# Kernel tuning notes

Measured on AMD Instinct MI355X. Metric: run time of the kernel, lower is better.

Reference implementation:

```python
import jax, jax.numpy as jnp
import numpy as np

EPS = 1e-5

def setup_inputs() -> dict:
    key = jax.random.key(0)
    ks = jax.random.split(key, 4)
    B, C, H, W = 32, 256, 32, 32
    x = jax.random.normal(ks[0], (B, C, H, W), dtype=jnp.float32)
    gamma = jnp.ones((C,), dtype=jnp.float32)
    beta = jnp.zeros((C,), dtype=jnp.float32)
    # torch nn.Linear init scale ~ 1/sqrt(fan_in)
    W_kqv = jax.random.normal(ks[1], (3 * C, C), dtype=jnp.float32) / np.sqrt(C)
    b_kqv = jnp.zeros((3 * C,), dtype=jnp.float32)
    W_proj = jax.random.normal(ks[2], (C, C), dtype=jnp.float32) / np.sqrt(C)
    b_proj = jnp.zeros((C,), dtype=jnp.float32)
    return {"x": x, "gamma": gamma, "beta": beta, "W_kqv": W_kqv,
            "b_kqv": b_kqv, "W_proj": W_proj, "b_proj": b_proj}

def reference(x, gamma, beta, W_kqv, b_kqv, W_proj, b_proj):
    B, C, H, W = x.shape
    scale = jnp.sqrt(jnp.asarray(C, dtype=x.dtype))
    # BatchNorm2d (training-mode batch statistics, biased variance, eps=1e-5)
    mean = jnp.mean(x, axis=(0, 2, 3), keepdims=True)
    var = jnp.var(x, axis=(0, 2, 3), keepdims=True)
    t = (x - mean) * jax.lax.rsqrt(var + EPS)
    t = t * gamma[None, :, None, None] + beta[None, :, None, None]
    # [B, C, H, W] -> [B, N, C] with N = H*W
    t = t.reshape(B, C, H * W).transpose(0, 2, 1)
    kqv = t @ W_kqv.T + b_kqv           # [B, N, 3C]
    q, k, v = jnp.split(kqv, 3, axis=-1)  # each [B, N, C]
    s = jnp.einsum('bnc,bmc->bnm', q, k) / scale  # [B, N, N]
    attn = jax.nn.softmax(s, axis=-1)
    o = jnp.einsum('bnm,bmc->bnc', attn, v)        # [B, N, C]
    o = o @ W_proj.T + b_proj
    o = o.transpose(0, 2, 1).reshape(B, C, H, W)
    return o + x
```

## Files before the change

kernel.cpp:

```cpp
#include <hip/hip_runtime.h>

typedef unsigned short u16;
typedef __attribute__((ext_vector_type(8))) short bf16x8;
typedef __attribute__((ext_vector_type(4))) float f32x4;

__device__ __forceinline__ float bf2f(u16 u) {
  union { unsigned u; float f; } c; c.u = ((unsigned)u) << 16; return c.f;
}
__device__ __forceinline__ u16 f2bf(float f) {
  union { float f; unsigned u; } c; c.f = f;
  unsigned u = c.u;
  return (u16)((u + 0x7FFFu + ((u >> 16) & 1u)) >> 16);
}
__device__ __forceinline__ void gld16(const void* g, void* l) {
  __builtin_amdgcn_global_load_lds(
      (__attribute__((address_space(1))) void*)g,
      (__attribute__((address_space(3))) void*)l, 16, 0, 0);
}

#define SYNCB() do { \
  asm volatile("s_waitcnt vmcnt(0) lgkmcnt(0)" ::: "memory"); \
  __builtin_amdgcn_s_barrier(); \
  __builtin_amdgcn_sched_barrier(0); \
} while (0)

#define BB 32
#define CC 256
#define NN 1024

__global__ __launch_bounds__(256) void bn_stats_kernel(
    const float* __restrict__ x, const float* __restrict__ gamma,
    const float* __restrict__ beta, float* __restrict__ scl, float* __restrict__ sft)
{
  int c = blockIdx.x;
  int tid = threadIdx.x;
  float s = 0.f, q = 0.f;
  for (int g = tid; g < 8192; g += 256) {
    int b = g >> 8;
    int n = (g & 255) * 4;
    float4 v = *reinterpret_cast<const float4*>(x + (((size_t)(b * CC + c)) << 10) + n);
    s += v.x + v.y + v.z + v.w;
    q += v.x * v.x + v.y * v.y + v.z * v.z + v.w * v.w;
  }
  __shared__ float rs[256], rq[256];
  rs[tid] = s; rq[tid] = q;
  __syncthreads();
  for (int off = 128; off > 0; off >>= 1) {
    if (tid < off) { rs[tid] += rs[tid + off]; rq[tid] += rq[tid + off]; }
    __syncthreads();
  }
  if (tid == 0) {
    float mean = rs[0] * (1.f / 32768.f);
    float var  = rq[0] * (1.f / 32768.f) - mean * mean;
    float rstd = rsqrtf(var + 1e-5f);
    float g = gamma[c] * rstd;
    scl[c] = g;
    sft[c] = beta[c] - mean * g;
  }
}

__global__ __launch_bounds__(256) void prep_w_kernel(
    const float* __restrict__ Wk, const float* __restrict__ bk,
    const float* __restrict__ Wp, const float* __restrict__ bp,
    const float* __restrict__ scl, const float* __restrict__ sft,
    u16* __restrict__ Wkb, float* __restrict__ bkbf,
    u16* __restrict__ Wpb, float* __restrict__ bpbf)
{
  int o = blockIdx.x, c = threadIdx.x;
  __shared__ float red[256];
  if (o < 768) {
    float w = Wk[o * 256 + c];
    Wkb[o * 256 + c] = f2bf(w * scl[c]);
    red[c] = w * sft[c];
    __syncthreads();
    for (int off = 128; off > 0; off >>= 1) {
      if (c < off) red[c] += red[c + off];
      __syncthreads();
    }
    if (c == 0) bkbf[o] = bk[o] + red[0];
  } else {
    int op = o - 768;
    Wpb[op * 256 + c] = f2bf(Wp[op * 256 + c]);
    if (c == 0) bpbf[op] = bp[op];
  }
}

__global__ __launch_bounds__(256, 2) void qkv_fused_kernel(
    const float* __restrict__ x, const u16* __restrict__ Wkb,
    const float* __restrict__ bkbf, u16* __restrict__ qkout, u16* __restrict__ vt)
{
  __shared__ __align__(16) u16 As[2][128 * 32];
  __shared__ __align__(16) u16 Bs[2][256 * 32];
  int bid = blockIdx.x;
  int bx = bid & 255, by = bid >> 8;
  int b = bx >> 3, nsp0 = (bx & 7) * 128;
  int tid = threadIdx.x, lane = tid & 63, w = tid >> 6;
  int lq = lane & 15, quad = lane >> 4;
  int wm = (w >> 1) * 64, wn = (w & 1) * 128;
  int ar = lane >> 2, ac = (lane & 3) * 8;
  int rbB = w * 64;
  int nn4 = (tid & 31) * 4;
  int c8i = tid >> 5;
  int cg  = c8i * 4;

  const float* xb = x + (((size_t)(b * CC)) << 10) + nsp0 + nn4;
  const u16* Bw = Wkb + (size_t)(by * 256) * 256;

  f32x4 zero = {0.f, 0.f, 0.f, 0.f};
  f32x4 acc[4][8];
  #pragma unroll
  for (int i = 0; i < 4; ++i)
    #pragma unroll
    for (int j = 0; j < 8; ++j) acc[i][j] = zero;

  float4 xA[4], xB[4];
  #pragma unroll
  for (int i = 0; i < 4; ++i)
    gld16(Bw + (size_t)(rbB + i * 16 + ar) * 256 + ac, &Bs[0][(rbB + i * 16) * 32]);
  #pragma unroll
  for (int ci = 0; ci < 4; ++ci)
    xA[ci] = *reinterpret_cast<const float4*>(xb + ((size_t)(cg + ci) << 10));

  auto body = [&](int t, float4 (&xc)[4], float4 (&xn)[4]) {
    int k0 = t * 32;
    if (t < 7) {
      int kn = k0 + 32;
      #pragma unroll
      for (int i = 0; i < 4; ++i)
        gld16(Bw + (size_t)(rbB + i * 16 + ar) * 256 + kn + ac,
              &Bs[(t + 1) & 1][(rbB + i * 16) * 32]);
      #pragma unroll
      for (int ci = 0; ci < 4; ++ci)
        xn[ci] = *reinterpret_cast<const float4*>(xb + ((size_t)(kn + cg + ci) << 10));
    }
    if (t < 7) {
      asm volatile("s_waitcnt vmcnt(8)" ::: "memory");
    } else {
      asm volatile("s_waitcnt vmcnt(0)" ::: "memory");
    }
    __builtin_amdgcn_sched_barrier(0);
    u16 av[4][4];
    #pragma unroll
    for (int ci = 0; ci < 4; ++ci) {
      av[ci][0] = f2bf(xc[ci].x);
      av[ci][1] = f2bf(xc[ci].y);
      av[ci][2] = f2bf(xc[ci].z);
      av[ci][3] = f2bf(xc[ci].w);
    }
    int c16 = c8i >> 1, lo8 = (c8i & 1) * 4;
    #pragma unroll
    for (int ni = 0; ni < 4; ++ni) {
      int n = nn4 + ni;
      int s2 = (n >> 2) & 3;
      ushort4 o4;
      o4.x = av[0][ni]; o4.y = av[1][ni]; o4.z = av[2][ni]; o4.w = av[3][ni];
      *reinterpret_cast<ushort4*>(
          &As[t & 1][n * 32 + ((c16 ^ s2) * 8 + lo8)]) = o4;
    }
    asm volatile("s_waitcnt lgkmcnt(0)" ::: "memory");
    __builtin_amdgcn_s_barrier();
    __builtin_amdgcn_sched_barrier(0);

    bf16x8 af[4], bfr[8];
    #pragma unroll
    for (int i = 0; i < 4; ++i) {
      int r = wm + i * 16 + lq;
      af[i] = *reinterpret_cast<const bf16x8*>(
          &As[t & 1][r * 32 + ((quad ^ ((r >> 2) & 3)) * 8)]);
    }
    #pragma unroll
    for (int j = 0; j < 8; ++j)
      bfr[j] = *reinterpret_cast<const bf16x8*>(
          &Bs[t & 1][(wn + j * 16 + lq) * 32 + quad * 8]);
    __builtin_amdgcn_s_setprio(1);
    #pragma unroll
    for (int i = 0; i < 4; ++i)
      #pragma unroll
      for (int j = 0; j < 8; ++j)
        acc[i][j] = __builtin_amdgcn_mfma_f32_16x16x32_bf16(af[i], bfr[j], acc[i][j], 0, 0, 0);
    __builtin_amdgcn_s_setprio(0);
    asm volatile("s_waitcnt lgkmcnt(0)" ::: "memory");
    __builtin_amdgcn_s_barrier();
    __builtin_amdgcn_sched_barrier(0);
  };

  #pragma unroll 1
  for (int tt = 0; tt < 4; ++tt) {
    body(2 * tt,     xA, xB);
    body(2 * tt + 1, xB, xA);
  }

  if (by < 2) {
    #pragma unroll
    for (int j = 0; j < 8; ++j) {
      int col = by * 256 + wn + j * 16 + lq;
      float bv = bkbf[col];
      #pragma unroll
      for (int i = 0; i < 4; ++i) {
        int m = (b << 10) + nsp0 + wm + i * 16 + quad * 4;
        #pragma unroll
        for (int r = 0; r < 4; ++r)
          qkout[(size_t)(m + r) * 512 + col] = f2bf(acc[i][j][r] + bv);
      }
    }
  } else {
    #pragma unroll
    for (int j = 0; j < 8; ++j) {
      int col = wn + j * 16 + lq;
      float bv = bkbf[512 + col];
      #pragma unroll
      for (int i = 0; i < 4; ++i) {
        int n = nsp0 + wm + i * 16 + quad * 4;
        ushort4 o;
        o.x = f2bf(acc[i][j][0] + bv);
        o.y = f2bf(acc[i][j][1] + bv);
        o.z = f2bf(acc[i][j][2] + bv);
        o.w = f2bf(acc[i][j][3] + bv);
        *reinterpret_cast<ushort4*>(&vt[(size_t)b * 262144 + (size_t)col * 1024 + n]) = o;
      }
    }
  }
}

__global__ __launch_bounds__(256) void gemm_nt_kernel(
    const u16* __restrict__ A, int lda, size_t sA,
    const u16* __restrict__ B, int ldb, size_t sB,
    u16* __restrict__ C, int ldc, size_t sC,
    int K, const float* __restrict__ bias, float scale, int mode,
    const float* __restrict__ xres, float* __restrict__ outf)
{
  __shared__ u16 As[128 * 32];
  __shared__ u16 Bs[128 * 32];
  int tid = threadIdx.x;
  int m0 = blockIdx.x * 128, n0 = blockIdx.y * 128;
  const u16* Ab = A + (size_t)blockIdx.z * sA;
  const u16* Bb = B + (size_t)blockIdx.z * sB;
  u16* Cb = C + (size_t)blockIdx.z * sC;

  int lane = tid & 63, w = tid >> 6;
  int lq = lane & 15, quad = lane >> 4;
  int wm = (w >> 1) * 64, wn = (w & 1) * 64;
  int ar = lane >> 2, ac = (lane & 3) * 8;
  int rb = w * 32;

  f32x4 zero = {0.f, 0.f, 0.f, 0.f};
  f32x4 acc[4][4];
  #pragma unroll
  for (int i = 0; i < 4; ++i)
    #pragma unroll
    for (int j = 0; j < 4; ++j) acc[i][j] = zero;

  for (int k0 = 0; k0 < K; k0 += 32) {
    __syncthreads();
    gld16(Ab + (size_t)(m0 + rb +      ar) * lda + k0 + ac, &As[(rb     ) * 32]);
    gld16(Ab + (size_t)(m0 + rb + 16 + ar) * lda + k0 + ac, &As[(rb + 16) * 32]);
    gld16(Bb + (size_t)(n0 + rb +      ar) * ldb + k0 + ac, &Bs[(rb     ) * 32]);
    gld16(Bb + (size_t)(n0 + rb + 16 + ar) * ldb + k0 + ac, &Bs[(rb + 16) * 32]);
    __syncthreads();
    bf16x8 af[4], bfr[4];
    #pragma unroll
    for (int i = 0; i < 4; ++i) {
      af[i]  = *reinterpret_cast<const bf16x8*>(&As[(wm + i * 16 + lq) * 32 + quad * 8]);
      bfr[i] = *reinterpret_cast<const bf16x8*>(&Bs[(wn + i * 16 + lq) * 32 + quad * 8]);
    }
    #pragma unroll
    for (int i = 0; i < 4; ++i)
      #pragma unroll
      for (int j = 0; j < 4; ++j)
        acc[i][j] = __builtin_amdgcn_mfma_f32_16x16x32_bf16(af[i], bfr[j], acc[i][j], 0, 0, 0);
  }

  #pragma unroll
  for (int j = 0; j < 4; ++j) {
    int col = n0 + wn + j * 16 + lq;
    float bv = bias ? bias[col] : 0.f;
    #pragma unroll
    for (int i = 0; i < 4; ++i) {
      int rbase = m0 + wm + i * 16 + quad * 4;
      if (mode == 2) {
        int b = rbase >> 10, n = rbase & 1023;
        size_t idx = (((size_t)(b * CC + col)) << 10) + n;
        float4 xv = *reinterpret_cast<const float4*>(xres + idx);
        float4 o;
        o.x = acc[i][j][0] * scale + bv + xv.x;
        o.y = acc[i][j][1] * scale + bv + xv.y;
        o.z = acc[i][j][2] * scale + bv + xv.z;
        o.w = acc[i][j][3] * scale + bv + xv.w;
        *reinterpret_cast<float4*>(outf + idx) = o;
      } else {
        #pragma unroll
        for (int r = 0; r < 4; ++r)
          Cb[(size_t)(rbase + r) * ldc + col] = f2bf(acc[i][j][r] * scale + bv);
      }
    }
  }
}

__global__ __launch_bounds__(512, 2) void attn_kernel(
    const u16* __restrict__ qk,
    const u16* __restrict__ vt,
    u16* __restrict__ o)
{
  __shared__ __align__(16) u16 Ks[2][64 * 256];
  __shared__ __align__(16) u16 Vs[2][256 * 64];
  __shared__ __align__(16) u16 Ps[128 * 64];
  float* rs = (float*)Ps;

  int bid = blockIdx.x;
  int b  = (bid & 7) + 8 * ((bid >> 3) & 3);
  int qt = bid >> 5;
  int tid = threadIdx.x, lane = tid & 63, w = tid >> 6;
  int lq = lane & 15, hh = lane >> 4;
  int wr = w & 3;
  bool isQK = w < 4;

  const u16* qb = qk + ((size_t)b << 10) * 512;
  const u16* kb = qb + 256;
  const u16* vb = vt + ((size_t)b << 18);

  auto stageK = [&](int kt, int bufi) {
    #pragma unroll
    for (int i = 0; i < 4; ++i) {
      int slot = i * 512 + tid;
      int r = slot >> 5, c = slot & 31;
      gld16(kb + (size_t)(kt * 64 + r) * 512 + ((c ^ (r & 7)) << 3),
            &Ks[bufi][(i * 512 + (tid & 448)) * 8]);
    }
  };
  auto stageV = [&](int kt, int bufi) {
    #pragma unroll
    for (int i = 0; i < 4; ++i) {
      int slot = i * 512 + tid;
      int n = slot >> 3, c = slot & 7;
      gld16(vb + (size_t)(n << 10) + kt * 64 + ((c ^ (n & 7)) << 3),
            &Vs[bufi][(i * 512 + (tid & 448)) * 8]);
    }
  };

  f32x4 zero = {0.f, 0.f, 0.f, 0.f};

  stageK(0, 0);
  SYNCB();

  if (isQK) {
    int q0 = qt * 128 + wr * 32;
    bf16x8 qf[2][8];
    #pragma unroll
    for (int qi = 0; qi < 2; ++qi)
      #pragma unroll
      for (int kk = 0; kk < 8; ++kk)
        qf[qi][kk] = *reinterpret_cast<const bf16x8*>(
            qb + (size_t)(q0 + qi * 16 + lq) * 512 + kk * 32 + hh * 8);
    float runsum[2][4] = {{0.f, 0.f, 0.f, 0.f}, {0.f, 0.f, 0.f, 0.f}};

    #pragma unroll 1
    for (int p = 0; p <= 16; ++p) {
      if (p <= 15) stageV(p, p & 1);
      if (p <= 14) stageK(p + 1, (p + 1) & 1);
      u16 pbv[2][4][4];
      if (p <= 15) {
        const u16* Kc = Ks[p & 1];
        f32x4 sacc[2][4];
        #pragma unroll
        for (int qi = 0; qi < 2; ++qi)
          #pragma unroll
          for (int ni = 0; ni < 4; ++ni) sacc[qi][ni] = zero;
        #pragma unroll
        for (int kk = 0; kk < 8; ++kk) {
          bf16x8 kf[4];
          #pragma unroll
          for (int ni = 0; ni < 4; ++ni) {
            int r = ni * 16 + lq;
            kf[ni] = *reinterpret_cast<const bf16x8*>(
                &Kc[r * 256 + (((kk * 4 + hh) ^ (r & 7)) << 3)]);
          }
          __builtin_amdgcn_s_setprio(1);
          #pragma unroll
          for (int qi = 0; qi < 2; ++qi)
            #pragma unroll
            for (int ni = 0; ni < 4; ++ni)
              sacc[qi][ni] = __builtin_amdgcn_mfma_f32_16x16x32_bf16(
                  qf[qi][kk], kf[ni], sacc[qi][ni], 0, 0, 0);
          __builtin_amdgcn_s_setprio(0);
        }
        #pragma unroll
        for (int qi = 0; qi < 2; ++qi)
          #pragma unroll
          for (int ni = 0; ni < 4; ++ni)
            #pragma unroll
            for (int rr = 0; rr < 4; ++rr) {
              float pexp = __expf(sacc[qi][ni][rr] * 0.0625f);
              u16 pb = f2bf(pexp);
              runsum[qi][rr] += bf2f(pb);
              pbv[qi][ni][rr] = pb;
            }
      }
      SYNCB();
      if (p <= 15) {
        #pragma unroll
        for (int qi = 0; qi < 2; ++qi)
          #pragma unroll
          for (int ni = 0; ni < 4; ++ni)
            #pragma unroll
            for (int rr = 0; rr < 4; ++rr) {
              int q = wr * 32 + qi * 16 + hh * 4 + rr;
              int kcol = ni * 16 + lq;
              Ps[q * 64 + ((((kcol >> 3) ^ (q & 7)) << 3) | (kcol & 7))] =
                  pbv[qi][ni][rr];
            }
      }
      SYNCB();
    }

    #pragma unroll
    for (int qi = 0; qi < 2; ++qi)
      #pragma unroll
      for (int rr = 0; rr < 4; ++rr) {
        float s = runsum[qi][rr];
        s += __shfl_xor(s, 1, 64);
        s += __shfl_xor(s, 2, 64);
        s += __shfl_xor(s, 4, 64);
        s += __shfl_xor(s, 8, 64);
        if (lq == 0) rs[wr * 32 + qi * 16 + hh * 4 + rr] = 1.f / s;
      }
    SYNCB();
  } else {
    f32x4 oacc[8][4];
    #pragma unroll
    for (int qi = 0; qi < 8; ++qi)
      #pragma unroll
      for (int nj = 0; nj < 4; ++nj) oacc[qi][nj] = zero;

    #pragma unroll 1
    for (int p = 0; p <= 16; ++p) {
      if (p <= 15) stageV(p, p & 1);
      if (p <= 14) stageK(p + 1, (p + 1) & 1);
      if (p >= 1) {
        const u16* Vc = Vs[(p - 1) & 1];
        #pragma unroll
        for (int kk2 = 0; kk2 < 2; ++kk2) {
          bf16x8 pa[8];
          #pragma unroll
          for (int qi = 0; qi < 8; ++qi) {
            int r = qi * 16 + lq;
            pa[qi] = *reinterpret_cast<const bf16x8*>(
                &Ps[r * 64 + (((kk2 * 4 + hh) ^ (r & 7)) << 3)]);
          }
          bf16x8 vf[4];
          #pragma unroll
          for (int nj = 0; nj < 4; ++nj) {
            int n = wr * 64 + nj * 16 + lq;
            vf[nj] = *reinterpret_cast<const bf16x8*>(
                &Vc[n * 64 + (((kk2 * 4 + hh) ^ (n & 7)) << 3)]);
          }
          __builtin_amdgcn_s_setprio(1);
          #pragma unroll
          for (int qi = 0; qi < 8; ++qi)
            #pragma unroll
            for (int nj = 0; nj < 4; ++nj)
              oacc[qi][nj] = __builtin_amdgcn_mfma_f32_16x16x32_bf16(
                  pa[qi], vf[nj], oacc[qi][nj], 0, 0, 0);
          __builtin_amdgcn_s_setprio(0);
        }
      }
      SYNCB();
      SYNCB();
    }

    SYNCB();
    float rinv[8][4];
    #pragma unroll
    for (int qi = 0; qi < 8; ++qi)
      #pragma unroll
      for (int rr = 0; rr < 4; ++rr)
        rinv[qi][rr] = rs[qi * 16 + hh * 4 + rr];
    u16* ob = o + ((size_t)(b << 10) + qt * 128) * 256;
    #pragma unroll
    for (int qi = 0; qi < 8; ++qi)
      #pragma unroll
      for (int nj = 0; nj < 4; ++nj)
        #pragma unroll
        for (int rr = 0; rr < 4; ++rr)
          ob[(size_t)(qi * 16 + hh * 4 + rr) * 256 + wr * 64 + nj * 16 + lq] =
              f2bf(oacc[qi][nj][rr] * rinv[qi][rr]);
  }
}

extern "C" void kernel_launch(void* const* d_in, const int* in_sizes, int n_in,
                              void* d_out, int out_size, void* d_ws, size_t ws_size,
                              hipStream_t stream) {
  const float* x     = (const float*)d_in[0];
  const float* gamma = (const float*)d_in[1];
  const float* beta  = (const float*)d_in[2];
  const float* Wkqv  = (const float*)d_in[3];
  const float* bkqv  = (const float*)d_in[4];
  const float* Wproj = (const float*)d_in[5];
  const float* bproj = (const float*)d_in[6];
  float* out = (float*)d_out;

  char* ws = (char*)d_ws;
  float* scl  = (float*)ws;
  float* sft  = (float*)(ws + 1024);
  u16* Wkb    = (u16*)(ws + 4096);
  u16* Wpb    = (u16*)(ws + 397312);
  float* bkbf = (float*)(ws + 528384);
  float* bpbf = (float*)(ws + 531456);
  u16* qk   = (u16*)(ws + 1048576);
  u16* vt   = qk + (size_t)32768 * 512;
  u16* o_pv = vt + (size_t)32 * 256 * 1024;

  bn_stats_kernel<<<dim3(256), dim3(256), 0, stream>>>(x, gamma, beta, scl, sft);
  prep_w_kernel<<<dim3(1024), dim3(256), 0, stream>>>(
      Wkqv, bkqv, Wproj, bproj, scl, sft, Wkb, bkbf, Wpb, bpbf);
  qkv_fused_kernel<<<dim3(768), dim3(256), 0, stream>>>(
      x, Wkb, bkbf, qk, vt);
  attn_kernel<<<dim3(256), dim3(512), 0, stream>>>(qk, vt, o_pv);
  gemm_nt_kernel<<<dim3(256, 2, 1), dim3(256), 0, stream>>>(
      o_pv, 256, 0, Wpb, 256, 0, nullptr, 0, 0, 256, bpbf, 1.0f, 2, x, out);
}
```

Measured before the change: 199.7 us.

## Double attention block to 16 waves, halving per-wave QK and PV tiles

```diff
diff --git a/kernel.cpp b/kernel.cpp
--- a/kernel.cpp
+++ b/kernel.cpp
@@ -296,7 +296,7 @@
   }
 }
 
-__global__ __launch_bounds__(512, 2) void attn_kernel(
+__global__ __launch_bounds__(1024, 4) void attn_kernel(
     const u16* __restrict__ qk,
     const u16* __restrict__ vt,
     u16* __restrict__ o)
@@ -311,8 +311,8 @@
   int qt = bid >> 5;
   int tid = threadIdx.x, lane = tid & 63, w = tid >> 6;
   int lq = lane & 15, hh = lane >> 4;
-  int wr = w & 3;
-  bool isQK = w < 4;
+  int wr = w & 7;
+  bool isQK = w < 8;
 
   const u16* qb = qk + ((size_t)b << 10) * 512;
   const u16* kb = qb + 256;
@@ -320,20 +320,20 @@
 
   auto stageK = [&](int kt, int bufi) {
     #pragma unroll
-    for (int i = 0; i < 4; ++i) {
-      int slot = i * 512 + tid;
+    for (int i = 0; i < 2; ++i) {
+      int slot = i * 1024 + tid;
       int r = slot >> 5, c = slot & 31;
       gld16(kb + (size_t)(kt * 64 + r) * 512 + ((c ^ (r & 7)) << 3),
-            &Ks[bufi][(i * 512 + (tid & 448)) * 8]);
+            &Ks[bufi][(i * 1024 + (tid & 960)) * 8]);
     }
   };
   auto stageV = [&](int kt, int bufi) {
     #pragma unroll
-    for (int i = 0; i < 4; ++i) {
-      int slot = i * 512 + tid;
+    for (int i = 0; i < 2; ++i) {
+      int slot = i * 1024 + tid;
       int n = slot >> 3, c = slot & 7;
       gld16(vb + (size_t)(n << 10) + kt * 64 + ((c ^ (n & 7)) << 3),
-            &Vs[bufi][(i * 512 + (tid & 448)) * 8]);
+            &Vs[bufi][(i * 1024 + (tid & 960)) * 8]);
     }
   };
 
@@ -343,28 +343,24 @@
   SYNCB();
 
   if (isQK) {
-    int q0 = qt * 128 + wr * 32;
-    bf16x8 qf[2][8];
-    #pragma unroll
-    for (int qi = 0; qi < 2; ++qi)
-      #pragma unroll
-      for (int kk = 0; kk < 8; ++kk)
-        qf[qi][kk] = *reinterpret_cast<const bf16x8*>(
-            qb + (size_t)(q0 + qi * 16 + lq) * 512 + kk * 32 + hh * 8);
-    float runsum[2][4] = {{0.f, 0.f, 0.f, 0.f}, {0.f, 0.f, 0.f, 0.f}};
+    int q0 = qt * 128 + wr * 16;
+    bf16x8 qf[8];
+    #pragma unroll
+    for (int kk = 0; kk < 8; ++kk)
+      qf[kk] = *reinterpret_cast<const bf16x8*>(
+          qb + (size_t)(q0 + lq) * 512 + kk * 32 + hh * 8);
+    float runsum[4] = {0.f, 0.f, 0.f, 0.f};
 
     #pragma unroll 1
     for (int p = 0; p <= 16; ++p) {
       if (p <= 15) stageV(p, p & 1);
       if (p <= 14) stageK(p + 1, (p + 1) & 1);
-      u16 pbv[2][4][4];
+      u16 pbv[4][4];
       if (p <= 15) {
         const u16* Kc = Ks[p & 1];
-        f32x4 sacc[2][4];
-        #pragma unroll
-        for (int qi = 0; qi < 2; ++qi)
-          #pragma unroll
-          for (int ni = 0; ni < 4; ++ni) sacc[qi][ni] = zero;
+        f32x4 sacc[4];
+        #pragma unroll
+        for (int ni = 0; ni < 4; ++ni) sacc[ni] = zero;
         #pragma unroll
         for (int kk = 0; kk < 8; ++kk) {
           bf16x8 kf[4];
@@ -376,58 +372,52 @@
           }
           __builtin_amdgcn_s_setprio(1);
           #pragma unroll
-          for (int qi = 0; qi < 2; ++qi)
-            #pragma unroll
-            for (int ni = 0; ni < 4; ++ni)
-              sacc[qi][ni] = __builtin_amdgcn_mfma_f32_16x16x32_bf16(
-                  qf[qi][kk], kf[ni], sacc[qi][ni], 0, 0, 0);
+          for (int ni = 0; ni < 4; ++ni)
+            sacc[ni] = __builtin_amdgcn_mfma_f32_16x16x32_bf16(
+                qf[kk], kf[ni], sacc[ni], 0, 0, 0);
           __builtin_amdgcn_s_setprio(0);
         }
         #pragma unroll
-        for (int qi = 0; qi < 2; ++qi)
-          #pragma unroll
-          for (int ni = 0; ni < 4; ++ni)
-            #pragma unroll
-            for (int rr = 0; rr < 4; ++rr) {
-              float pexp = __expf(sacc[qi][ni][rr] * 0.0625f);
-              u16 pb = f2bf(pexp);
-              runsum[qi][rr] += bf2f(pb);
-              pbv[qi][ni][rr] = pb;
-            }
+        for (int ni = 0; ni < 4; ++ni)
+          #pragma unroll
+          for (int rr = 0; rr < 4; ++rr) {
+            float pexp = __expf(sacc[ni][rr] * 0.0625f);
+            u16 pb = f2bf(pexp);
+            runsum[rr] += bf2f(pb);
+            pbv[ni][rr] = pb;
+          }
       }
       SYNCB();
       if (p <= 15) {
         #pragma unroll
-        for (int qi = 0; qi < 2; ++qi)
-          #pragma unroll
-          for (int ni = 0; ni < 4; ++ni)
-            #pragma unroll
-            for (int rr = 0; rr < 4; ++rr) {
-              int q = wr * 32 + qi * 16 + hh * 4 + rr;
-              int kcol = ni * 16 + lq;
-              Ps[q * 64 + ((((kcol >> 3) ^ (q & 7)) << 3) | (kcol & 7))] =
-                  pbv[qi][ni][rr];
-            }
+        for (int ni = 0; ni < 4; ++ni)
+          #pragma unroll
+          for (int rr = 0; rr < 4; ++rr) {
+            int q = wr * 16 + hh * 4 + rr;
+            int kcol = ni * 16 + lq;
+            Ps[q * 64 + ((((kcol >> 3) ^ (q & 7)) << 3) | (kcol & 7))] =
+                pbv[ni][rr];
+          }
       }
       SYNCB();
     }
 
     #pragma unroll
-    for (int qi = 0; qi < 2; ++qi)
-      #pragma unroll
-      for (int rr = 0; rr < 4; ++rr) {
-        float s = runsum[qi][rr];
-        s += __shfl_xor(s, 1, 64);
-        s += __shfl_xor(s, 2, 64);
-        s += __shfl_xor(s, 4, 64);
-        s += __shfl_xor(s, 8, 64);
-        if (lq == 0) rs[wr * 32 + qi * 16 + hh * 4 + rr] = 1.f / s;
-      }
+    for (int rr = 0; rr < 4; ++rr) {
+      float s = runsum[rr];
+      s += __shfl_xor(s, 1, 64);
+      s += __shfl_xor(s, 2, 64);
+      s += __shfl_xor(s, 4, 64);
+      s += __shfl_xor(s, 8, 64);
+      if (lq == 0) rs[wr * 16 + hh * 4 + rr] = 1.f / s;
+    }
     SYNCB();
   } else {
-    f32x4 oacc[8][4];
-    #pragma unroll
-    for (int qi = 0; qi < 8; ++qi)
+    int rh = (wr >> 2) * 64;
+    int wc = (wr & 3) * 64;
+    f32x4 oacc[4][4];
+    #pragma unroll
+    for (int qi = 0; qi < 4; ++qi)
       #pragma unroll
       for (int nj = 0; nj < 4; ++nj) oacc[qi][nj] = zero;
 
@@ -439,23 +429,23 @@
         const u16* Vc = Vs[(p - 1) & 1];
         #pragma unroll
         for (int kk2 = 0; kk2 < 2; ++kk2) {
-          bf16x8 pa[8];
-          #pragma unroll
-          for (int qi = 0; qi < 8; ++qi) {
-            int r = qi * 16 + lq;
+          bf16x8 pa[4];
+          #pragma unroll
+          for (int qi = 0; qi < 4; ++qi) {
+            int r = rh + qi * 16 + lq;
             pa[qi] = *reinterpret_cast<const bf16x8*>(
                 &Ps[r * 64 + (((kk2 * 4 + hh) ^ (r & 7)) << 3)]);
           }
           bf16x8 vf[4];
           #pragma unroll
           for (int nj = 0; nj < 4; ++nj) {
-            int n = wr * 64 + nj * 16 + lq;
+            int n = wc + nj * 16 + lq;
             vf[nj] = *reinterpret_cast<const bf16x8*>(
                 &Vc[n * 64 + (((kk2 * 4 + hh) ^ (n & 7)) << 3)]);
           }
           __builtin_amdgcn_s_setprio(1);
           #pragma unroll
-          for (int qi = 0; qi < 8; ++qi)
+          for (int qi = 0; qi < 4; ++qi)
             #pragma unroll
             for (int nj = 0; nj < 4; ++nj)
               oacc[qi][nj] = __builtin_amdgcn_mfma_f32_16x16x32_bf16(
@@ -468,20 +458,20 @@
     }
 
     SYNCB();
-    float rinv[8][4];
-    #pragma unroll
-    for (int qi = 0; qi < 8; ++qi)
+    float rinv[4][4];
+    #pragma unroll
+    for (int qi = 0; qi < 4; ++qi)
       #pragma unroll
       for (int rr = 0; rr < 4; ++rr)
-        rinv[qi][rr] = rs[qi * 16 + hh * 4 + rr];
+        rinv[qi][rr] = rs[rh + qi * 16 + hh * 4 + rr];
     u16* ob = o + ((size_t)(b << 10) + qt * 128) * 256;
     #pragma unroll
-    for (int qi = 0; qi < 8; ++qi)
+    for (int qi = 0; qi < 4; ++qi)
       #pragma unroll
       for (int nj = 0; nj < 4; ++nj)
         #pragma unroll
         for (int rr = 0; rr < 4; ++rr)
-          ob[(size_t)(qi * 16 + hh * 4 + rr) * 256 + wr * 64 + nj * 16 + lq] =
+          ob[(size_t)(rh + qi * 16 + hh * 4 + rr) * 256 + wc + nj * 16 + lq] =
               f2bf(oacc[qi][nj][rr] * rinv[qi][rr]);
   }
 }
@@ -514,7 +504,7 @@
       Wkqv, bkqv, Wproj, bproj, scl, sft, Wkb, bkbf, Wpb, bpbf);
   qkv_fused_kernel<<<dim3(768), dim3(256), 0, stream>>>(
       x, Wkb, bkbf, qk, vt);
-  attn_kernel<<<dim3(256), dim3(512), 0, stream>>>(qk, vt, o_pv);
+  attn_kernel<<<dim3(256), dim3(1024), 0, stream>>>(qk, vt, o_pv);
   gemm_nt_kernel<<<dim3(256, 2, 1), dim3(256), 0, stream>>>(
       o_pv, 256, 0, Wpb, 256, 0, nullptr, 0, 0, 256, bpbf, 1.0f, 2, x, out);
 }
```

Result: no change. 201.0 us (+0.7%).

## Split BN stats across blocks with atomics; double-buffer projection GEMM

Applied to the files above, without the earlier changes.

```diff
diff --git a/kernel.cpp b/kernel.cpp
--- a/kernel.cpp
+++ b/kernel.cpp
@@ -29,49 +29,61 @@
 #define NN 1024
 
 __global__ __launch_bounds__(256) void bn_stats_kernel(
-    const float* __restrict__ x, const float* __restrict__ gamma,
-    const float* __restrict__ beta, float* __restrict__ scl, float* __restrict__ sft)
+    const float* __restrict__ x, float* __restrict__ ssum, float* __restrict__ qsum)
 {
-  int c = blockIdx.x;
+  int bid = blockIdx.x;
+  int c = bid & 255, slice = bid >> 8;
   int tid = threadIdx.x;
+  float4 v[4];
+  #pragma unroll
+  for (int i = 0; i < 4; ++i) {
+    int g = i * 256 + tid;
+    int b = slice * 4 + (g >> 8);
+    int n = (g & 255) * 4;
+    v[i] = *reinterpret_cast<const float4*>(x + (((size_t)(b * CC + c)) << 10) + n);
+  }
   float s = 0.f, q = 0.f;
-  for (int g = tid; g < 8192; g += 256) {
-    int b = g >> 8;
-    int n = (g & 255) * 4;
-    float4 v = *reinterpret_cast<const float4*>(x + (((size_t)(b * CC + c)) << 10) + n);
-    s += v.x + v.y + v.z + v.w;
-    q += v.x * v.x + v.y * v.y + v.z * v.z + v.w * v.w;
-  }
-  __shared__ float rs[256], rq[256];
-  rs[tid] = s; rq[tid] = q;
+  #pragma unroll
+  for (int i = 0; i < 4; ++i) {
+    s += v[i].x + v[i].y + v[i].z + v[i].w;
+    q += v[i].x * v[i].x + v[i].y * v[i].y + v[i].z * v[i].z + v[i].w * v[i].w;
+  }
+  #pragma unroll
+  for (int off = 32; off > 0; off >>= 1) {
+    s += __shfl_down(s, off, 64);
+    q += __shfl_down(q, off, 64);
+  }
+  __shared__ float rs[4], rq[4];
+  int w = tid >> 6, lane = tid & 63;
+  if (lane == 0) { rs[w] = s; rq[w] = q; }
   __syncthreads();
-  for (int off = 128; off > 0; off >>= 1) {
-    if (tid < off) { rs[tid] += rs[tid + off]; rq[tid] += rq[tid + off]; }
-    __syncthreads();
-  }
   if (tid == 0) {
-    float mean = rs[0] * (1.f / 32768.f);
-    float var  = rq[0] * (1.f / 32768.f) - mean * mean;
-    float rstd = rsqrtf(var + 1e-5f);
-    float g = gamma[c] * rstd;
-    scl[c] = g;
-    sft[c] = beta[c] - mean * g;
+    float st = rs[0] + rs[1] + rs[2] + rs[3];
+    float qt = rq[0] + rq[1] + rq[2] + rq[3];
+    atomicAdd(&ssum[c], st);
+    atomicAdd(&qsum[c], qt);
   }
 }
 
 __global__ __launch_bounds__(256) void prep_w_kernel(
     const float* __restrict__ Wk, const float* __restrict__ bk,
     const float* __restrict__ Wp, const float* __restrict__ bp,
-    const float* __restrict__ scl, const float* __restrict__ sft,
+    const float* __restrict__ gamma, const float* __restrict__ beta,
+    const float* __restrict__ ssum, const float* __restrict__ qsum,
     u16* __restrict__ Wkb, float* __restrict__ bkbf,
     u16* __restrict__ Wpb, float* __restrict__ bpbf)
 {
   int o = blockIdx.x, c = threadIdx.x;
   __shared__ float red[256];
   if (o < 768) {
+    float mean = ssum[c] * (1.f / 32768.f);
+    float var  = qsum[c] * (1.f / 32768.f) - mean * mean;
+    float rstd = rsqrtf(var + 1e-5f);
+    float g    = gamma[c] * rstd;
+    float sftc = beta[c] - mean * g;
     float w = Wk[o * 256 + c];
-    Wkb[o * 256 + c] = f2bf(w * scl[c]);
-    red[c] = w * sft[c];
+    Wkb[o * 256 + c] = f2bf(w * g);
+    red[c] = w * sftc;
     __syncthreads();
     for (int off = 128; off > 0; off >>= 1) {
       if (c < off) red[c] += red[c + off];
@@ -222,21 +234,15 @@
   }
 }
 
-__global__ __launch_bounds__(256) void gemm_nt_kernel(
-    const u16* __restrict__ A, int lda, size_t sA,
-    const u16* __restrict__ B, int ldb, size_t sB,
-    u16* __restrict__ C, int ldc, size_t sC,
-    int K, const float* __restrict__ bias, float scale, int mode,
-    const float* __restrict__ xres, float* __restrict__ outf)
+__global__ __launch_bounds__(256, 2) void proj_kernel(
+    const u16* __restrict__ A, const u16* __restrict__ Bw,
+    const float* __restrict__ bias, const float* __restrict__ xres,
+    float* __restrict__ outf)
 {
-  __shared__ u16 As[128 * 32];
-  __shared__ u16 Bs[128 * 32];
+  __shared__ __align__(16) u16 As[2][128 * 32];
+  __shared__ __align__(16) u16 Bs[2][128 * 32];
   int tid = threadIdx.x;
   int m0 = blockIdx.x * 128, n0 = blockIdx.y * 128;
-  const u16* Ab = A + (size_t)blockIdx.z * sA;
-  const u16* Bb = B + (size_t)blockIdx.z * sB;
-  u16* Cb = C + (size_t)blockIdx.z * sC;
-
   int lane = tid & 63, w = tid >> 6;
   int lq = lane & 15, quad = lane >> 4;
   int wm = (w >> 1) * 64, wn = (w & 1) * 64;
@@ -250,48 +256,60 @@
     #pragma unroll
     for (int j = 0; j < 4; ++j) acc[i][j] = zero;
 
-  for (int k0 = 0; k0 < K; k0 += 32) {
-    __syncthreads();
-    gld16(Ab + (size_t)(m0 + rb +      ar) * lda + k0 + ac, &As[(rb     ) * 32]);
-    gld16(Ab + (size_t)(m0 + rb + 16 + ar) * lda + k0 + ac, &As[(rb + 16) * 32]);
-    gld16(Bb + (size_t)(n0 + rb +      ar) * ldb + k0 + ac, &Bs[(rb     ) * 32]);
-    gld16(Bb + (size_t)(n0 + rb + 16 + ar) * ldb + k0 + ac, &Bs[(rb + 16) * 32]);
-    __syncthreads();
+  auto stage = [&](int k0, int bufi) {
+    gld16(A  + (size_t)(m0 + rb +      ar) * 256 + k0 + ac, &As[bufi][(rb     ) * 32]);
+    gld16(A  + (size_t)(m0 + rb + 16 + ar) * 256 + k0 + ac, &As[bufi][(rb + 16) * 32]);
+    gld16(Bw + (size_t)(n0 + rb +      ar) * 256 + k0 + ac, &Bs[bufi][(rb     ) * 32]);
+    gld16(Bw + (size_t)(n0 + rb + 16 + ar) * 256 + k0 + ac, &Bs[bufi][(rb + 16) * 32]);
+  };
+
+  stage(0, 0);
+
+  #pragma unroll 1
+  for (int t = 0; t < 8; ++t) {
+    if (t < 7) stage((t + 1) * 32, (t + 1) & 1);
+    if (t < 7) {
+      asm volatile("s_waitcnt vmcnt(4)" ::: "memory");
+    } else {
+      asm volatile("s_waitcnt vmcnt(0)" ::: "memory");
+    }
+    __builtin_amdgcn_sched_barrier(0);
+    __builtin_amdgcn_s_barrier();
+    __builtin_amdgcn_sched_barrier(0);
     bf16x8 af[4], bfr[4];
     #pragma unroll
     for (int i = 0; i < 4; ++i) {
-      af[i]  = *reinterpret_cast<const bf16x8*>(&As[(wm + i * 16 + lq) * 32 + quad * 8]);
-      bfr[i] = *reinterpret_cast<const bf16x8*>(&Bs[(wn + i * 16 + lq) * 32 + quad * 8]);
-    }
+      af[i]  = *reinterpret_cast<const bf16x8*>(&As[t & 1][(wm + i * 16 + lq) * 32 + quad * 8]);
+      bfr[i] = *reinterpret_cast<const bf16x8*>(&Bs[t & 1][(wn + i * 16 + lq) * 32 + quad * 8]);
+    }
+    __builtin_amdgcn_s_setprio(1);
     #pragma unroll
     for (int i = 0; i < 4; ++i)
       #pragma unroll
       for (int j = 0; j < 4; ++j)
         acc[i][j] = __builtin_amdgcn_mfma_f32_16x16x32_bf16(af[i], bfr[j], acc[i][j], 0, 0, 0);
+    __builtin_amdgcn_s_setprio(0);
+    asm volatile("s_waitcnt lgkmcnt(0)" ::: "memory");
+    __builtin_amdgcn_s_barrier();
+    __builtin_amdgcn_sched_barrier(0);
   }
 
   #pragma unroll
   for (int j = 0; j < 4; ++j) {
     int col = n0 + wn + j * 16 + lq;
-    float bv = bias ? bias[col] : 0.f;
+    float bv = bias[col];
     #pragma unroll
     for (int i = 0; i < 4; ++i) {
       int rbase = m0 + wm + i * 16 + quad * 4;
-      if (mode == 2) {
-        int b = rbase >> 10, n = rbase & 1023;
-        size_t idx = (((size_t)(b * CC + col)) << 10) + n;
-        float4 xv = *reinterpret_cast<const float4*>(xres + idx);
-        float4 o;
-        o.x = acc[i][j][0] * scale + bv + xv.x;
-        o.y = acc[i][j][1] * scale + bv + xv.y;
-        o.z = acc[i][j][2] * scale + bv + xv.z;
-        o.w = acc[i][j][3] * scale + bv + xv.w;
-        *reinterpret_cast<float4*>(outf + idx) = o;
-      } else {
-        #pragma unroll
-        for (int r = 0; r < 4; ++r)
-          Cb[(size_t)(rbase + r) * ldc + col] = f2bf(acc[i][j][r] * scale + bv);
-      }
+      int b = rbase >> 10, n = rbase & 1023;
+      size_t idx = (((size_t)(b * CC + col)) << 10) + n;
+      float4 xv = *reinterpret_cast<const float4*>(xres + idx);
+      float4 o;
+      o.x = acc[i][j][0] + bv + xv.x;
+      o.y = acc[i][j][1] + bv + xv.y;
+      o.z = acc[i][j][2] + bv + xv.z;
+      o.w = acc[i][j][3] + bv + xv.w;
+      *reinterpret_cast<float4*>(outf + idx) = o;
     }
   }
 }
@@ -499,22 +517,23 @@
   float* out = (float*)d_out;
 
   char* ws = (char*)d_ws;
-  float* scl  = (float*)ws;
-  float* sft  = (float*)(ws + 1024);
   u16* Wkb    = (u16*)(ws + 4096);
   u16* Wpb    = (u16*)(ws + 397312);
   float* bkbf = (float*)(ws + 528384);
   float* bpbf = (float*)(ws + 531456);
+  float* ssum = (float*)(ws + 540672);
+  float* qsum = (float*)(ws + 541696);
   u16* qk   = (u16*)(ws + 1048576);
   u16* vt   = qk + (size_t)32768 * 512;
   u16* o_pv = vt + (size_t)32 * 256 * 1024;
 
-  bn_stats_kernel<<<dim3(256), dim3(256), 0, stream>>>(x, gamma, beta, scl, sft);
+  hipMemsetAsync(ssum, 0, 2 * 256 * sizeof(float), stream);
+  bn_stats_kernel<<<dim3(2048), dim3(256), 0, stream>>>(x, ssum, qsum);
   prep_w_kernel<<<dim3(1024), dim3(256), 0, stream>>>(
-      Wkqv, bkqv, Wproj, bproj, scl, sft, Wkb, bkbf, Wpb, bpbf);
+      Wkqv, bkqv, Wproj, bproj, gamma, beta, ssum, qsum, Wkb, bkbf, Wpb, bpbf);
   qkv_fused_kernel<<<dim3(768), dim3(256), 0, stream>>>(
       x, Wkb, bkbf, qk, vt);
   attn_kernel<<<dim3(256), dim3(512), 0, stream>>>(qk, vt, o_pv);
-  gemm_nt_kernel<<<dim3(256, 2, 1), dim3(256), 0, stream>>>(
-      o_pv, 256, 0, Wpb, 256, 0, nullptr, 0, 0, 256, bpbf, 1.0f, 2, x, out);
-}
+  proj_kernel<<<dim3(256, 2), dim3(256), 0, stream>>>(
+      o_pv, Wpb, bpbf, x, out);
+}
```

Measured after the change: 195.1 us. -2.3%, faster.
